# Optimization experiments

Measured on AMD Instinct MI355X. Metric: run time of the kernel, lower is better.

Reference implementation:

```python
import jax, jax.numpy as jnp
import numpy as np

I_DIM = 50000
D_DIM = 128
N_EDGES = 800000
N_NODES = I_DIM + 1


def setup_inputs() -> dict:
    key = jax.random.key(0)
    k1, k2, k3, k4 = jax.random.split(key, 4)
    # edge[:,0] must be sorted for the original bincount+repeat normalization to be valid
    src = jnp.sort(jax.random.randint(k1, (N_EDGES,), 0, N_NODES))
    dst = jax.random.randint(k2, (N_EDGES,), 0, N_NODES)
    edge = jnp.stack([src, dst], axis=1).astype(jnp.int64)
    # GlorotNormal-style init for the embedding table and dense layers
    emb_mat = jax.random.normal(k3, (N_NODES, D_DIM), dtype=jnp.float32) * np.sqrt(2.0 / (N_NODES + D_DIM))
    kA, kB = jax.random.split(k4)
    W_scale = jax.random.normal(kA, (D_DIM, D_DIM), dtype=jnp.float32) * np.sqrt(2.0 / (2 * D_DIM))
    b_scale = jnp.zeros((D_DIM,), dtype=jnp.float32)
    W_att = jax.random.normal(kB, (2 * D_DIM, 1), dtype=jnp.float32) * np.sqrt(2.0 / (2 * D_DIM + 1))
    b_att = jnp.zeros((1,), dtype=jnp.float32)
    return {"edge": edge, "emb_mat": emb_mat, "W_scale": W_scale,
            "b_scale": b_scale, "W_att": W_att, "b_att": b_att}


def reference(edge, emb_mat, W_scale, b_scale, W_att, b_att):
    E = edge.shape[0]
    src = edge[:, 0]
    dst = edge[:, 1]
    # gather both endpoints, project: [E, 2, d]
    edge_emb = jnp.einsum('epd,df->epf', emb_mat[edge], W_scale) + b_scale
    edge_emb = edge_emb.reshape(E, -1)                       # [E, 2d]
    att = edge_emb @ W_att + b_att                           # [E, 1]
    att = jnp.where(att >= 0, att, 0.2 * att)                # LeakyReLU(0.2)
    att = jnp.squeeze(att, axis=-1)                          # [E]
    scores = jnp.exp(att - 1.0)
    score_sum = jax.ops.segment_sum(scores, src, num_segments=N_NODES)
    score_norm = scores / score_sum[src]                     # segment softmax
    item_scaled = emb_mat @ W_scale + b_scale                # [N, d]
    msgs = score_norm[:, None] * item_scaled[dst]            # [E, d]
    agg = jax.ops.segment_sum(msgs, src, num_segments=N_NODES)
    return jax.nn.sigmoid(agg)                               # [N, d]
```

## Files before the change

kernel.cpp:

```cpp
#include <hip/hip_runtime.h>
#include <math.h>


#define NN 50001
#define DD 128
#define NE 800000
#define EDGE_BLOCKS 3125
#define ATT_BLOCKS 3126
#define OUT_BLOCKS 782
#define TR_BLOCKS 64

typedef __attribute__((ext_vector_type(8))) short short8;
typedef __attribute__((ext_vector_type(4))) float floatx4;

__device__ __forceinline__ unsigned short f2bf(float f) {
    unsigned u = __builtin_bit_cast(unsigned, f);
    u += 0x7fffu + ((u >> 16) & 1u);
    return (unsigned short)(u >> 16);
}
__device__ __forceinline__ float bflo(unsigned u) {
    return __builtin_bit_cast(float, u << 16);
}
__device__ __forceinline__ float bfhi(unsigned u) {
    return __builtin_bit_cast(float, u & 0xffff0000u);
}
__device__ __forceinline__ float score(float att) {
    att = att >= 0.f ? att : 0.2f * att;
    return __expf(att - 1.f);
}

__global__ void __launch_bounds__(256) k_pre(const float* __restrict__ W,
        const float* __restrict__ W_att, const float* __restrict__ b_scale,
        const float* __restrict__ b_att, const int* __restrict__ edge,
        unsigned short* __restrict__ WT, float* __restrict__ u_src,
        float* __restrict__ u_dst, float* __restrict__ cb,
        int* __restrict__ row_ptr) {
    if (blockIdx.x < TR_BLOCKS) {
        int j = blockIdx.x * 2 + (threadIdx.x >> 7);
        int k = threadIdx.x & 127;
        WT[j * DD + k] = f2bf(W[k * DD + j]);
        return;
    }
    if (blockIdx.x == TR_BLOCKS) {
        int k = threadIdx.x;
        if (k < DD) {
            float us = 0.f, ud = 0.f;
            for (int j = 0; j < DD; j++) {
                float w = W[k * DD + j];
                us += w * W_att[j];
                ud += w * W_att[DD + j];
            }
            u_src[k] = us; u_dst[k] = ud;
        } else if (k == DD) {
            float c = b_att[0];
            for (int j = 0; j < DD; j++) c += b_scale[j] * W_att[j];
            cb[0] = c;
        } else if (k == DD + 1) {
            float c = 0.f;
            for (int j = 0; j < DD; j++) c += b_scale[j] * W_att[DD + j];
            cb[1] = c;
        }
        return;
    }
    int e = (blockIdx.x - TR_BLOCKS - 1) * 256 + threadIdx.x;
    if (e >= NE) return;
    int s = edge[2 * e];
    if (e == 0) {
        for (int n = 0; n <= s; n++) row_ptr[n] = 0;
    } else {
        int p = edge[2 * (e - 1)];
        for (int n = p + 1; n <= s; n++) row_ptr[n] = e;
    }
    if (e == NE - 1) {
        for (int n = s + 1; n <= NN; n++) row_ptr[n] = NE;
    }
}

__global__ void __launch_bounds__(256) k_att(const float* __restrict__ emb,
        const float* __restrict__ u_src, const float* __restrict__ u_dst,
        const float* __restrict__ cb, unsigned short* __restrict__ emb_bf,
        float* __restrict__ a_src, float* __restrict__ a_dst) {
    int n = blockIdx.x * 16 + (threadIdx.x >> 4);
    int t = threadIdx.x & 15;
    if (n >= NN) return;

    const float* ep = emb + (long)n * DD + t * 8;
    float4 e0 = *(const float4*)(ep);
    float4 e1 = *(const float4*)(ep + 4);
    float4 us0 = *(const float4*)(u_src + t * 8);
    float4 us1 = *(const float4*)(u_src + t * 8 + 4);
    float4 ud0 = *(const float4*)(u_dst + t * 8);
    float4 ud1 = *(const float4*)(u_dst + t * 8 + 4);

    float ps = e0.x * us0.x + e0.y * us0.y + e0.z * us0.z + e0.w * us0.w
             + e1.x * us1.x + e1.y * us1.y + e1.z * us1.z + e1.w * us1.w;
    float pd = e0.x * ud0.x + e0.y * ud0.y + e0.z * ud0.z + e0.w * ud0.w
             + e1.x * ud1.x + e1.y * ud1.y + e1.z * ud1.z + e1.w * ud1.w;

    uint4 pk;
    pk.x = (unsigned)f2bf(e0.x) | ((unsigned)f2bf(e0.y) << 16);
    pk.y = (unsigned)f2bf(e0.z) | ((unsigned)f2bf(e0.w) << 16);
    pk.z = (unsigned)f2bf(e1.x) | ((unsigned)f2bf(e1.y) << 16);
    pk.w = (unsigned)f2bf(e1.z) | ((unsigned)f2bf(e1.w) << 16);
    *(uint4*)(emb_bf + (long)n * DD + t * 8) = pk;

    ps += __shfl_xor(ps, 1, 16); ps += __shfl_xor(ps, 2, 16);
    ps += __shfl_xor(ps, 4, 16); ps += __shfl_xor(ps, 8, 16);
    pd += __shfl_xor(pd, 1, 16); pd += __shfl_xor(pd, 2, 16);
    pd += __shfl_xor(pd, 4, 16); pd += __shfl_xor(pd, 8, 16);
    if (t == 0) { a_src[n] = ps + cb[0]; a_dst[n] = pd + cb[1]; }
}

#define ACC8(S, U) \
    acc[0] += (S) * bflo((U).x); acc[1] += (S) * bfhi((U).x); \
    acc[2] += (S) * bflo((U).y); acc[3] += (S) * bfhi((U).y); \
    acc[4] += (S) * bflo((U).z); acc[5] += (S) * bfhi((U).z); \
    acc[6] += (S) * bflo((U).w); acc[7] += (S) * bfhi((U).w);

__global__ void __launch_bounds__(256) k_agg(const int* __restrict__ edge,
        const int* __restrict__ row_ptr, const unsigned short* __restrict__ emb_bf,
        const float* __restrict__ a_src, const float* __restrict__ a_dst,
        unsigned short* __restrict__ aggN) {
    int n = blockIdx.x * 16 + (threadIdx.x >> 4);
    int t = threadIdx.x & 15;
    if (n >= NN) return;

    int start = row_ptr[n];
    int len = row_ptr[n + 1] - start;
    unsigned short* op = aggN + (long)n * DD + t * 8;

    if (len <= 0) {
        uint4 z = make_uint4(0u, 0u, 0u, 0u);
        *(uint4*)op = z;
        return;
    }

    float asrc = a_src[n];
    const int* dp = edge + 2 * start + 1;
    const unsigned short* ip = emb_bf + t * 8;

    float acc[8] = {0.f, 0.f, 0.f, 0.f, 0.f, 0.f, 0.f, 0.f};
    float ssum = 0.f;

    for (int j = 0; j < len; j += 16) {
        int jj = j + t;
        int idx = jj < len ? jj : len - 1;
        int d = dp[2 * idx];
        float x = a_dst[d];
        float s = (jj < len) ? score(asrc + x) : 0.f;
        ssum += s;

        int cnt = len - j;
        if (cnt > 16) cnt = 16;
        int kk = 0;
        for (; kk + 4 <= cnt; kk += 4) {
            int d0 = __shfl(d, kk, 16),     d1 = __shfl(d, kk + 1, 16);
            int d2 = __shfl(d, kk + 2, 16), d3 = __shfl(d, kk + 3, 16);
            float s0 = __shfl(s, kk, 16),     s1 = __shfl(s, kk + 1, 16);
            float s2 = __shfl(s, kk + 2, 16), s3 = __shfl(s, kk + 3, 16);
            uint4 u0 = *(const uint4*)(ip + (long)d0 * DD);
            uint4 u1 = *(const uint4*)(ip + (long)d1 * DD);
            uint4 u2 = *(const uint4*)(ip + (long)d2 * DD);
            uint4 u3 = *(const uint4*)(ip + (long)d3 * DD);
            ACC8(s0, u0);
            ACC8(s1, u1);
            ACC8(s2, u2);
            ACC8(s3, u3);
        }
        for (; kk < cnt; kk++) {
            int d0 = __shfl(d, kk, 16);
            float s0 = __shfl(s, kk, 16);
            uint4 u0 = *(const uint4*)(ip + (long)d0 * DD);
            ACC8(s0, u0);
        }
    }

    ssum += __shfl_xor(ssum, 1, 16);
    ssum += __shfl_xor(ssum, 2, 16);
    ssum += __shfl_xor(ssum, 4, 16);
    ssum += __shfl_xor(ssum, 8, 16);
    float inv = 1.f / ssum;

    uint4 pk;
    pk.x = (unsigned)f2bf(acc[0] * inv) | ((unsigned)f2bf(acc[1] * inv) << 16);
    pk.y = (unsigned)f2bf(acc[2] * inv) | ((unsigned)f2bf(acc[3] * inv) << 16);
    pk.z = (unsigned)f2bf(acc[4] * inv) | ((unsigned)f2bf(acc[5] * inv) << 16);
    pk.w = (unsigned)f2bf(acc[6] * inv) | ((unsigned)f2bf(acc[7] * inv) << 16);
    *(uint4*)op = pk;
}

__global__ void __launch_bounds__(256) k_out(const unsigned short* __restrict__ aggN,
        const unsigned short* __restrict__ WT, const float* __restrict__ b_scale,
        const int* __restrict__ row_ptr, float* __restrict__ out) {
    int wave = blockIdx.x * 4 + (threadIdx.x >> 6);
    int lane = threadIdx.x & 63;
    int base = wave * 16;
    if (base >= NN) return;
    int m = lane & 15, q = lane >> 4;
    int node = base + m;
    bool valid = node < NN;
    int row = valid ? node : NN - 1;
    int len = row_ptr[row + 1] - row_ptr[row];

    const unsigned short* bp = aggN + (long)row * DD + q * 8;
    short8 b[4];
    #pragma unroll
    for (int ks = 0; ks < 4; ks++)
        b[ks] = *(const short8*)(bp + ks * 32);

    #pragma unroll
    for (int ft = 0; ft < 8; ft++) {
        floatx4 acc = {0.f, 0.f, 0.f, 0.f};
        const unsigned short* wrow = WT + (ft * 16 + m) * DD + q * 8;
        #pragma unroll
        for (int ks = 0; ks < 4; ks++) {
            short8 a = *(const short8*)(wrow + ks * 32);
            acc = __builtin_amdgcn_mfma_f32_16x16x32_bf16(a, b[ks], acc, 0, 0, 0);
        }
        if (valid) {
            int fo = ft * 16 + q * 4;
            float4 bs = *(const float4*)(b_scale + fo);
            float4 o;
            if (len > 0) {
                o.x = 1.f / (1.f + __expf(-(acc[0] + bs.x)));
                o.y = 1.f / (1.f + __expf(-(acc[1] + bs.y)));
                o.z = 1.f / (1.f + __expf(-(acc[2] + bs.z)));
                o.w = 1.f / (1.f + __expf(-(acc[3] + bs.w)));
            } else {
                o = make_float4(0.5f, 0.5f, 0.5f, 0.5f);
            }
            *(float4*)(out + (long)node * DD + fo) = o;
        }
    }
}

extern "C" void kernel_launch(void* const* d_in, const int* in_sizes, int n_in,
                              void* d_out, int out_size, void* d_ws, size_t ws_size,
                              hipStream_t stream) {
    const int*   edge    = (const int*)d_in[0];
    const float* emb     = (const float*)d_in[1];
    const float* W_scale = (const float*)d_in[2];
    const float* b_scale = (const float*)d_in[3];
    const float* W_att   = (const float*)d_in[4];
    const float* b_att   = (const float*)d_in[5];
    float* out = (float*)d_out;

    char* ws = (char*)d_ws;
    int*            row_ptr = (int*)(ws);
    float*          a_src   = (float*)(ws + 200832);
    float*          a_dst   = (float*)(ws + 401024);
    unsigned short* emb_bf  = (unsigned short*)(ws + 601216);
    unsigned short* aggN    = (unsigned short*)(ws + 13401472);
    unsigned short* WT      = (unsigned short*)(ws + 26201728);
    float*          u_src   = (float*)(ws + 26234496);
    float*          u_dst   = (float*)(ws + 26235008);
    float*          cb      = (float*)(ws + 26235520);

    k_pre <<<TR_BLOCKS + 1 + EDGE_BLOCKS, 256, 0, stream>>>(W_scale, W_att, b_scale,
                                                            b_att, edge, WT, u_src,
                                                            u_dst, cb, row_ptr);
    k_att <<<ATT_BLOCKS,  256, 0, stream>>>(emb, u_src, u_dst, cb, emb_bf,
                                            a_src, a_dst);
    k_agg <<<ATT_BLOCKS,  256, 0, stream>>>(edge, row_ptr, emb_bf, a_src, a_dst,
                                            aggN);
    k_out <<<OUT_BLOCKS,  256, 0, stream>>>(aggN, WT, b_scale, row_ptr, out);
}
```

Baseline: 145.6 us.

## Fuse edge aggregation with output projection through shared memory

Merges the aggregation kernel and the MFMA projection/sigmoid kernel into one: each 256-thread block aggregates 16 nodes into a padded shared-memory tile, syncs, then its four waves each compute two 16-column output tiles. This removes the bf16 aggN round trip through global memory and one kernel launch. It also widens the gather inner loop to 8 outstanding row loads. In exchange, WT is now reloaded by all ~3126 blocks instead of 782, and a block barrier makes waves wait for the slowest node's aggregation.

Result: faster. 141.0 us (-3.1%).

```diff
diff --git a/kernel.cpp b/kernel.cpp
--- a/kernel.cpp
+++ b/kernel.cpp
@@ -7,8 +7,8 @@
 #define NE 800000
 #define EDGE_BLOCKS 3125
 #define ATT_BLOCKS 3126
-#define OUT_BLOCKS 782
 #define TR_BLOCKS 64
+#define ASTRIDE 136
 
 typedef __attribute__((ext_vector_type(8))) short short8;
 typedef __attribute__((ext_vector_type(4))) float floatx4;
@@ -117,99 +117,110 @@
     acc[4] += (S) * bflo((U).z); acc[5] += (S) * bfhi((U).z); \
     acc[6] += (S) * bflo((U).w); acc[7] += (S) * bfhi((U).w);
 
-__global__ void __launch_bounds__(256) k_agg(const int* __restrict__ edge,
+__global__ void __launch_bounds__(256) k_fused(const int* __restrict__ edge,
         const int* __restrict__ row_ptr, const unsigned short* __restrict__ emb_bf,
         const float* __restrict__ a_src, const float* __restrict__ a_dst,
-        unsigned short* __restrict__ aggN) {
-    int n = blockIdx.x * 16 + (threadIdx.x >> 4);
-    int t = threadIdx.x & 15;
-    if (n >= NN) return;
-
-    int start = row_ptr[n];
-    int len = row_ptr[n + 1] - start;
-    unsigned short* op = aggN + (long)n * DD + t * 8;
-
-    if (len <= 0) {
-        uint4 z = make_uint4(0u, 0u, 0u, 0u);
-        *(uint4*)op = z;
-        return;
-    }
-
-    float asrc = a_src[n];
-    const int* dp = edge + 2 * start + 1;
-    const unsigned short* ip = emb_bf + t * 8;
-
-    float acc[8] = {0.f, 0.f, 0.f, 0.f, 0.f, 0.f, 0.f, 0.f};
-    float ssum = 0.f;
-
-    for (int j = 0; j < len; j += 16) {
-        int jj = j + t;
-        int idx = jj < len ? jj : len - 1;
-        int d = dp[2 * idx];
-        float x = a_dst[d];
-        float s = (jj < len) ? score(asrc + x) : 0.f;
-        ssum += s;
-
-        int cnt = len - j;
-        if (cnt > 16) cnt = 16;
-        int kk = 0;
-        for (; kk + 4 <= cnt; kk += 4) {
-            int d0 = __shfl(d, kk, 16),     d1 = __shfl(d, kk + 1, 16);
-            int d2 = __shfl(d, kk + 2, 16), d3 = __shfl(d, kk + 3, 16);
-            float s0 = __shfl(s, kk, 16),     s1 = __shfl(s, kk + 1, 16);
-            float s2 = __shfl(s, kk + 2, 16), s3 = __shfl(s, kk + 3, 16);
-            uint4 u0 = *(const uint4*)(ip + (long)d0 * DD);
-            uint4 u1 = *(const uint4*)(ip + (long)d1 * DD);
-            uint4 u2 = *(const uint4*)(ip + (long)d2 * DD);
-            uint4 u3 = *(const uint4*)(ip + (long)d3 * DD);
-            ACC8(s0, u0);
-            ACC8(s1, u1);
-            ACC8(s2, u2);
-            ACC8(s3, u3);
-        }
-        for (; kk < cnt; kk++) {
-            int d0 = __shfl(d, kk, 16);
-            float s0 = __shfl(s, kk, 16);
-            uint4 u0 = *(const uint4*)(ip + (long)d0 * DD);
-            ACC8(s0, u0);
-        }
-    }
-
-    ssum += __shfl_xor(ssum, 1, 16);
-    ssum += __shfl_xor(ssum, 2, 16);
-    ssum += __shfl_xor(ssum, 4, 16);
-    ssum += __shfl_xor(ssum, 8, 16);
-    float inv = 1.f / ssum;
-
-    uint4 pk;
-    pk.x = (unsigned)f2bf(acc[0] * inv) | ((unsigned)f2bf(acc[1] * inv) << 16);
-    pk.y = (unsigned)f2bf(acc[2] * inv) | ((unsigned)f2bf(acc[3] * inv) << 16);
-    pk.z = (unsigned)f2bf(acc[4] * inv) | ((unsigned)f2bf(acc[5] * inv) << 16);
-    pk.w = (unsigned)f2bf(acc[6] * inv) | ((unsigned)f2bf(acc[7] * inv) << 16);
-    *(uint4*)op = pk;
-}
-
-__global__ void __launch_bounds__(256) k_out(const unsigned short* __restrict__ aggN,
         const unsigned short* __restrict__ WT, const float* __restrict__ b_scale,
-        const int* __restrict__ row_ptr, float* __restrict__ out) {
-    int wave = blockIdx.x * 4 + (threadIdx.x >> 6);
+        float* __restrict__ out) {
+    __shared__ unsigned short AGG[16 * ASTRIDE];
+    __shared__ int LENS[16];
+
+    int g = threadIdx.x >> 4, t = threadIdx.x & 15;
+    int n = blockIdx.x * 16 + g;
+    bool nvalid = n < NN;
+
+    int start = 0, len = 0;
+    if (nvalid) { start = row_ptr[n]; len = row_ptr[n + 1] - start; }
+    if (t == 0) LENS[g] = nvalid ? len : 0;
+
+    uint4 pk = make_uint4(0u, 0u, 0u, 0u);
+    if (nvalid && len > 0) {
+        float asrc = a_src[n];
+        const int* dp = edge + 2 * start + 1;
+        const unsigned short* ip = emb_bf + t * 8;
+
+        float acc[8] = {0.f, 0.f, 0.f, 0.f, 0.f, 0.f, 0.f, 0.f};
+        float ssum = 0.f;
+
+        for (int j = 0; j < len; j += 16) {
+            int jj = j + t;
+            int idx = jj < len ? jj : len - 1;
+            int d = dp[2 * idx];
+            float x = a_dst[d];
+            float s = (jj < len) ? score(asrc + x) : 0.f;
+            ssum += s;
+
+            int cnt = len - j;
+            if (cnt > 16) cnt = 16;
+            int kk = 0;
+            for (; kk + 8 <= cnt; kk += 8) {
+                int d0 = __shfl(d, kk, 16),     d1 = __shfl(d, kk + 1, 16);
+                int d2 = __shfl(d, kk + 2, 16), d3 = __shfl(d, kk + 3, 16);
+                int d4 = __shfl(d, kk + 4, 16), d5 = __shfl(d, kk + 5, 16);
+                int d6 = __shfl(d, kk + 6, 16), d7 = __shfl(d, kk + 7, 16);
+                float s0 = __shfl(s, kk, 16),     s1 = __shfl(s, kk + 1, 16);
+                float s2 = __shfl(s, kk + 2, 16), s3 = __shfl(s, kk + 3, 16);
+                float s4 = __shfl(s, kk + 4, 16), s5 = __shfl(s, kk + 5, 16);
+                float s6 = __shfl(s, kk + 6, 16), s7 = __shfl(s, kk + 7, 16);
+                uint4 u0 = *(const uint4*)(ip + (long)d0 * DD);
+                uint4 u1 = *(const uint4*)(ip + (long)d1 * DD);
+                uint4 u2 = *(const uint4*)(ip + (long)d2 * DD);
+                uint4 u3 = *(const uint4*)(ip + (long)d3 * DD);
+                uint4 u4 = *(const uint4*)(ip + (long)d4 * DD);
+                uint4 u5 = *(const uint4*)(ip + (long)d5 * DD);
+                uint4 u6 = *(const uint4*)(ip + (long)d6 * DD);
+                uint4 u7 = *(const uint4*)(ip + (long)d7 * DD);
+                ACC8(s0, u0); ACC8(s1, u1); ACC8(s2, u2); ACC8(s3, u3);
+                ACC8(s4, u4); ACC8(s5, u5); ACC8(s6, u6); ACC8(s7, u7);
+            }
+            for (; kk + 4 <= cnt; kk += 4) {
+                int d0 = __shfl(d, kk, 16),     d1 = __shfl(d, kk + 1, 16);
+                int d2 = __shfl(d, kk + 2, 16), d3 = __shfl(d, kk + 3, 16);
+                float s0 = __shfl(s, kk, 16),     s1 = __shfl(s, kk + 1, 16);
+                float s2 = __shfl(s, kk + 2, 16), s3 = __shfl(s, kk + 3, 16);
+                uint4 u0 = *(const uint4*)(ip + (long)d0 * DD);
+                uint4 u1 = *(const uint4*)(ip + (long)d1 * DD);
+                uint4 u2 = *(const uint4*)(ip + (long)d2 * DD);
+                uint4 u3 = *(const uint4*)(ip + (long)d3 * DD);
+                ACC8(s0, u0); ACC8(s1, u1); ACC8(s2, u2); ACC8(s3, u3);
+            }
+            for (; kk < cnt; kk++) {
+                int d0 = __shfl(d, kk, 16);
+                float s0 = __shfl(s, kk, 16);
+                uint4 u0 = *(const uint4*)(ip + (long)d0 * DD);
+                ACC8(s0, u0);
+            }
+        }
+
+        ssum += __shfl_xor(ssum, 1, 16);
+        ssum += __shfl_xor(ssum, 2, 16);
+        ssum += __shfl_xor(ssum, 4, 16);
+        ssum += __shfl_xor(ssum, 8, 16);
+        float inv = 1.f / ssum;
+
+        pk.x = (unsigned)f2bf(acc[0] * inv) | ((unsigned)f2bf(acc[1] * inv) << 16);
+        pk.y = (unsigned)f2bf(acc[2] * inv) | ((unsigned)f2bf(acc[3] * inv) << 16);
+        pk.z = (unsigned)f2bf(acc[4] * inv) | ((unsigned)f2bf(acc[5] * inv) << 16);
+        pk.w = (unsigned)f2bf(acc[6] * inv) | ((unsigned)f2bf(acc[7] * inv) << 16);
+    }
+    *(uint4*)(AGG + g * ASTRIDE + t * 8) = pk;
+    __syncthreads();
+
+    int wave = threadIdx.x >> 6;
     int lane = threadIdx.x & 63;
-    int base = wave * 16;
-    if (base >= NN) return;
     int m = lane & 15, q = lane >> 4;
-    int node = base + m;
+    int node = blockIdx.x * 16 + m;
     bool valid = node < NN;
-    int row = valid ? node : NN - 1;
-    int len = row_ptr[row + 1] - row_ptr[row];
-
-    const unsigned short* bp = aggN + (long)row * DD + q * 8;
+    int lenm = LENS[m];
+
     short8 b[4];
     #pragma unroll
     for (int ks = 0; ks < 4; ks++)
-        b[ks] = *(const short8*)(bp + ks * 32);
+        b[ks] = *(const short8*)(AGG + m * ASTRIDE + ks * 32 + q * 8);
 
     #pragma unroll
-    for (int ft = 0; ft < 8; ft++) {
+    for (int f2 = 0; f2 < 2; f2++) {
+        int ft = wave * 2 + f2;
         floatx4 acc = {0.f, 0.f, 0.f, 0.f};
         const unsigned short* wrow = WT + (ft * 16 + m) * DD + q * 8;
         #pragma unroll
@@ -221,7 +232,7 @@
             int fo = ft * 16 + q * 4;
             float4 bs = *(const float4*)(b_scale + fo);
             float4 o;
-            if (len > 0) {
+            if (lenm > 0) {
                 o.x = 1.f / (1.f + __expf(-(acc[0] + bs.x)));
                 o.y = 1.f / (1.f + __expf(-(acc[1] + bs.y)));
                 o.z = 1.f / (1.f + __expf(-(acc[2] + bs.z)));
@@ -250,18 +261,16 @@
     float*          a_src   = (float*)(ws + 200832);
     float*          a_dst   = (float*)(ws + 401024);
     unsigned short* emb_bf  = (unsigned short*)(ws + 601216);
-    unsigned short* aggN    = (unsigned short*)(ws + 13401472);
-    unsigned short* WT      = (unsigned short*)(ws + 26201728);
-    float*          u_src   = (float*)(ws + 26234496);
-    float*          u_dst   = (float*)(ws + 26235008);
-    float*          cb      = (float*)(ws + 26235520);
-
-    k_pre <<<TR_BLOCKS + 1 + EDGE_BLOCKS, 256, 0, stream>>>(W_scale, W_att, b_scale,
-                                                            b_att, edge, WT, u_src,
-                                                            u_dst, cb, row_ptr);
-    k_att <<<ATT_BLOCKS,  256, 0, stream>>>(emb, u_src, u_dst, cb, emb_bf,
-                                            a_src, a_dst);
-    k_agg <<<ATT_BLOCKS,  256, 0, stream>>>(edge, row_ptr, emb_bf, a_src, a_dst,
-                                            aggN);
-    k_out <<<OUT_BLOCKS,  256, 0, stream>>>(aggN, WT, b_scale, row_ptr, out);
-}
+    unsigned short* WT      = (unsigned short*)(ws + 13401472);
+    float*          u_src   = (float*)(ws + 13434240);
+    float*          u_dst   = (float*)(ws + 13434752);
+    float*          cb      = (float*)(ws + 13435264);
+
+    k_pre   <<<TR_BLOCKS + 1 + EDGE_BLOCKS, 256, 0, stream>>>(W_scale, W_att, b_scale,
+                                                              b_att, edge, WT, u_src,
+                                                              u_dst, cb, row_ptr);
+    k_att   <<<ATT_BLOCKS, 256, 0, stream>>>(emb, u_src, u_dst, cb, emb_bf,
+                                             a_src, a_dst);
+    k_fused <<<ATT_BLOCKS, 256, 0, stream>>>(edge, row_ptr, emb_bf, a_src, a_dst,
+                                             WT, b_scale, out);
+}
```
